# Optimization experiments

Hardware: AMD Instinct MI355X
Metric: run time of the kernel (lower is better)

## Reference

```python
import jax, jax.numpy as jnp
import numpy as np

N_NODES = 100000
N_EDGES = 1600000
IN_DIM = 64
HID = 128
OUT_DIM = 2
N_GRAPHS = 64


def setup_inputs() -> dict:
    key = jax.random.key(0)
    ks = jax.random.split(key, 9)
    x = jax.random.normal(ks[0], (N_NODES, IN_DIM), dtype=jnp.float32)
    edge_index = jax.random.randint(ks[1], (2, N_EDGES), 0, N_NODES, dtype=jnp.int64)
    batch = jnp.sort(jax.random.randint(ks[2], (N_NODES,), 0, N_GRAPHS, dtype=jnp.int64))
    # GCNConv weights (Glorot-ish scale) and biases
    W1 = jax.random.normal(ks[3], (IN_DIM, HID), dtype=jnp.float32) / np.sqrt(IN_DIM)
    b1 = jnp.zeros((HID,), dtype=jnp.float32)
    W2 = jax.random.normal(ks[4], (HID, HID), dtype=jnp.float32) / np.sqrt(HID)
    b2 = jnp.zeros((HID,), dtype=jnp.float32)
    Wfc = jax.random.normal(ks[5], (HID, OUT_DIM), dtype=jnp.float32) / np.sqrt(HID)
    bfc = jnp.zeros((OUT_DIM,), dtype=jnp.float32)
    return {"x": x, "W1": W1, "b1": b1, "W2": W2, "b2": b2,
            "Wfc": Wfc, "bfc": bfc, "edge_index": edge_index, "batch": batch}


def _gcn_conv(x, W, b, src, dst, num_nodes):
    # PyG GCNConv: linear transform, add self loops, symmetric deg norm, scatter-add.
    h = x @ W  # [N, F]
    loop = jnp.arange(num_nodes, dtype=src.dtype)
    s = jnp.concatenate([src, loop])  # source (message origin)
    d = jnp.concatenate([dst, loop])  # target (aggregation)
    deg = jax.ops.segment_sum(jnp.ones_like(d, dtype=h.dtype), d, num_segments=num_nodes)
    dinv = jnp.where(deg > 0, jax.lax.rsqrt(deg), 0.0)
    norm = dinv[s] * dinv[d]  # [E+N]
    msg = h[s] * norm[:, None]
    out = jax.ops.segment_sum(msg, d, num_segments=num_nodes)
    return out + b


def reference(x, W1, b1, W2, b2, Wfc, bfc, edge_index, batch):
    src, dst = edge_index[0], edge_index[1]
    n = x.shape[0]
    h = jax.nn.relu(_gcn_conv(x, W1, b1, src, dst, n))
    # dropout is a no-op in eval mode
    h = jax.nn.relu(_gcn_conv(h, W2, b2, src, dst, n))
    # global mean pool over graphs
    sums = jax.ops.segment_sum(h, batch, num_segments=N_GRAPHS)
    cnts = jax.ops.segment_sum(jnp.ones((n,), dtype=h.dtype), batch, num_segments=N_GRAPHS)
    pooled = sums / jnp.maximum(cnts, 1.0)[:, None]  # [G, HID]
    logits = pooled @ Wfc + bfc
    return jax.nn.log_softmax(logits, axis=1)
```

## Files before the change

kernel.cpp:

```cpp
#include <hip/hip_runtime.h>
#include <math.h>

#define N_NODES 100000
#define N_EDGES 1600000
#define IN_DIM 64
#define HID 128
#define OUT_DIM 2
#define N_GRAPHS 64

#define NBUK ((N_NODES + 255) / 256)
#define BCAP 4608
#define E4 (N_EDGES / 4)
#define NBLK_P1 ((E4 + 1023) / 1024)

#define PCHUNK 256
#define MAXCH 8

typedef unsigned int uint32;
typedef __attribute__((ext_vector_type(8))) short bf16x8;
typedef __attribute__((ext_vector_type(4))) float f32x4;

static __device__ __forceinline__ ushort f2bf(float f) {
    uint32 u = __float_as_uint(f);
    uint32 r = (u + 0x7fff + ((u >> 16) & 1)) >> 16;
    return (ushort)r;
}
static __device__ __forceinline__ float bf2f(uint32 u) {
    return __uint_as_float(u << 16);
}
static __device__ __forceinline__ float bflo(uint32 u) { return bf2f(u & 0xffffu); }
static __device__ __forceinline__ float bfhi(uint32 u) { return bf2f(u >> 16); }

__global__ __launch_bounds__(1024) void k_pass1(const int4* __restrict__ src4,
                                                const int4* __restrict__ dst4,
                                                int* __restrict__ gcur,
                                                int* __restrict__ bsrc,
                                                int* __restrict__ bdst) {
    __shared__ int hist[NBUK];
    __shared__ int base[NBUK];
    int tid = threadIdx.x;
    if (tid < NBUK) hist[tid] = 0;
    __syncthreads();
    int i4 = blockIdx.x * 1024 + tid;
    bool act = i4 < E4;
    int4 d = {0, 0, 0, 0}, s = {0, 0, 0, 0};
    if (act) {
        d = dst4[i4];
        s = src4[i4];
        atomicAdd(&hist[d.x >> 8], 1);
        atomicAdd(&hist[d.y >> 8], 1);
        atomicAdd(&hist[d.z >> 8], 1);
        atomicAdd(&hist[d.w >> 8], 1);
    }
    __syncthreads();
    if (tid < NBUK) {
        int c = hist[tid];
        base[tid] = tid * BCAP + (c ? atomicAdd(&gcur[tid], c) : 0);
        hist[tid] = 0;
    }
    __syncthreads();
    if (act) {
        int b0 = d.x >> 8, r0 = atomicAdd(&hist[b0], 1);
        int b1 = d.y >> 8, r1 = atomicAdd(&hist[b1], 1);
        int b2 = d.z >> 8, r2 = atomicAdd(&hist[b2], 1);
        int b3 = d.w >> 8, r3 = atomicAdd(&hist[b3], 1);
        int sl0 = base[b0] + r0;
        int sl1 = base[b1] + r1;
        int sl2 = base[b2] + r2;
        int sl3 = base[b3] + r3;
        bsrc[sl0] = s.x; bdst[sl0] = d.x;
        bsrc[sl1] = s.y; bdst[sl1] = d.y;
        bsrc[sl2] = s.z; bdst[sl2] = d.z;
        bsrc[sl3] = s.w; bdst[sl3] = d.w;
    }
}

__global__ __launch_bounds__(512) void k_bscan(const int* __restrict__ gcur,
                                               int* __restrict__ bstart,
                                               int* __restrict__ row_start) {
    __shared__ int s[512];
    int t = threadIdx.x;
    int v = (t < NBUK) ? gcur[t] : 0;
    s[t] = v;
    __syncthreads();
    for (int off = 1; off < 512; off <<= 1) {
        int u = (t >= off) ? s[t - off] : 0;
        __syncthreads();
        s[t] += u;
        __syncthreads();
    }
    if (t < NBUK) bstart[t] = s[t] - v;
    if (t == 0) row_start[N_NODES] = N_EDGES;
}

__global__ __launch_bounds__(1024) void k_pass2(const int* __restrict__ gcur,
                                                const int* __restrict__ bstart,
                                                const int* __restrict__ bsrc,
                                                const int* __restrict__ bdst,
                                                const float* __restrict__ x,
                                                int* __restrict__ row_start,
                                                float* __restrict__ dinv,
                                                int* __restrict__ csr,
                                                ushort* __restrict__ xs) {
    __shared__ int cnt[256];
    __shared__ int sc[256];
    __shared__ int lst[256];
    __shared__ float sdinv[256];
    int b = blockIdx.x;
    int tid = threadIdx.x;
    int node0 = b * 256;
    int nloc = N_NODES - node0;
    if (nloc > 256) nloc = 256;
    int bbase = b * BCAP;
    int Eb = gcur[b];

    if (tid < 256) cnt[tid] = 0;
    __syncthreads();
    for (int i = tid; i < Eb; i += 1024) atomicAdd(&cnt[bdst[bbase + i] & 255], 1);
    __syncthreads();
    int v = 0;
    if (tid < 256) {
        v = cnt[tid];
        sc[tid] = v;
    }
    __syncthreads();
    for (int off = 1; off < 256; off <<= 1) {
        int u = 0;
        if (tid < 256 && tid >= off) u = sc[tid - off];
        __syncthreads();
        if (tid < 256) sc[tid] += u;
        __syncthreads();
    }
    int gb = bstart[b];
    if (tid < 256) {
        int excl = sc[tid] - v;
        lst[tid] = excl;
        if (tid < nloc) {
            float dv = rsqrtf((float)(v + 1));
            row_start[node0 + tid] = gb + excl;
            dinv[node0 + tid] = dv;
            sdinv[tid] = dv;
        }
        cnt[tid] = 0;
    }
    __syncthreads();
    for (int i = tid; i < Eb; i += 1024) {
        int d = bdst[bbase + i];
        int s = bsrc[bbase + i];
        int dl = d & 255;
        int r = atomicAdd(&cnt[dl], 1);
        csr[gb + lst[dl] + r] = s;
    }
    int f0 = node0 * 16;
    int f1 = (node0 + nloc) * 16;
    for (int idx = f0 + tid; idx < f1; idx += 1024) {
        float dv = sdinv[(idx >> 4) - node0];
        float4 vv = ((const float4*)x)[idx];
        ushort4 o;
        o.x = f2bf(vv.x * dv);
        o.y = f2bf(vv.y * dv);
        o.z = f2bf(vv.z * dv);
        o.w = f2bf(vv.w * dv);
        ((ushort4*)xs)[idx] = o;
    }
}

__global__ __launch_bounds__(256) void k_gbound(const int* __restrict__ batch,
                                                int* __restrict__ gstart) {
    int n = blockIdx.x * 256 + threadIdx.x;
    if (n >= N_NODES) return;
    if (n == 0) {
        for (int g = 0; g <= batch[0]; ++g) gstart[g] = 0;
    } else {
        int a = batch[n - 1], b = batch[n];
        for (int g = a + 1; g <= b; ++g) gstart[g] = n;
    }
    if (n == N_NODES - 1) {
        for (int g = batch[n] + 1; g <= N_GRAPHS; ++g) gstart[g] = N_NODES;
    }
}

__global__ __launch_bounds__(256) void k_agg1(const int* __restrict__ row_start,
                                              const int* __restrict__ csr,
                                              const uint32* __restrict__ xs,
                                              const float* __restrict__ dinv,
                                              uint32* __restrict__ outb) {
    int d = blockIdx.x * 8 + (threadIdx.x >> 5);
    int l = threadIdx.x & 31;
    float dd = dinv[d];
    uint32 u = xs[(long long)d * 32 + l];
    float a0 = bflo(u), a1 = bfhi(u);
    int e = row_start[d];
    int eend = row_start[d + 1];
    for (; e + 7 < eend; e += 8) {
        int s0 = csr[e], s1 = csr[e + 1], s2 = csr[e + 2], s3 = csr[e + 3];
        int s4 = csr[e + 4], s5 = csr[e + 5], s6 = csr[e + 6], s7 = csr[e + 7];
        uint32 w0 = xs[(long long)s0 * 32 + l];
        uint32 w1 = xs[(long long)s1 * 32 + l];
        uint32 w2 = xs[(long long)s2 * 32 + l];
        uint32 w3 = xs[(long long)s3 * 32 + l];
        uint32 w4 = xs[(long long)s4 * 32 + l];
        uint32 w5 = xs[(long long)s5 * 32 + l];
        uint32 w6 = xs[(long long)s6 * 32 + l];
        uint32 w7 = xs[(long long)s7 * 32 + l];
        a0 += ((bflo(w0) + bflo(w1)) + (bflo(w2) + bflo(w3))) +
              ((bflo(w4) + bflo(w5)) + (bflo(w6) + bflo(w7)));
        a1 += ((bfhi(w0) + bfhi(w1)) + (bfhi(w2) + bfhi(w3))) +
              ((bfhi(w4) + bfhi(w5)) + (bfhi(w6) + bfhi(w7)));
    }
    for (; e + 3 < eend; e += 4) {
        int s0 = csr[e], s1 = csr[e + 1], s2 = csr[e + 2], s3 = csr[e + 3];
        uint32 w0 = xs[(long long)s0 * 32 + l];
        uint32 w1 = xs[(long long)s1 * 32 + l];
        uint32 w2 = xs[(long long)s2 * 32 + l];
        uint32 w3 = xs[(long long)s3 * 32 + l];
        a0 += (bflo(w0) + bflo(w1)) + (bflo(w2) + bflo(w3));
        a1 += (bfhi(w0) + bfhi(w1)) + (bfhi(w2) + bfhi(w3));
    }
    for (; e < eend; ++e) {
        uint32 w = xs[(long long)csr[e] * 32 + l];
        a0 += bflo(w);
        a1 += bfhi(w);
    }
    outb[(long long)d * 32 + l] = (uint32)f2bf(a0 * dd) | ((uint32)f2bf(a1 * dd) << 16);
}

__global__ __launch_bounds__(256) void k_agg2(const int* __restrict__ row_start,
                                              const int* __restrict__ csr,
                                              const uint2* __restrict__ hs,
                                              const float* __restrict__ dinv,
                                              uint2* __restrict__ outb) {
    int d = blockIdx.x * 8 + (threadIdx.x >> 5);
    int l = threadIdx.x & 31;
    float dd = dinv[d];
    uint2 u = hs[(long long)d * 32 + l];
    float a0 = bflo(u.x), a1 = bfhi(u.x), a2 = bflo(u.y), a3 = bfhi(u.y);
    int e = row_start[d];
    int eend = row_start[d + 1];
    for (; e + 7 < eend; e += 8) {
        int s0 = csr[e], s1 = csr[e + 1], s2 = csr[e + 2], s3 = csr[e + 3];
        int s4 = csr[e + 4], s5 = csr[e + 5], s6 = csr[e + 6], s7 = csr[e + 7];
        uint2 w0 = hs[(long long)s0 * 32 + l];
        uint2 w1 = hs[(long long)s1 * 32 + l];
        uint2 w2 = hs[(long long)s2 * 32 + l];
        uint2 w3 = hs[(long long)s3 * 32 + l];
        uint2 w4 = hs[(long long)s4 * 32 + l];
        uint2 w5 = hs[(long long)s5 * 32 + l];
        uint2 w6 = hs[(long long)s6 * 32 + l];
        uint2 w7 = hs[(long long)s7 * 32 + l];
        a0 += ((bflo(w0.x) + bflo(w1.x)) + (bflo(w2.x) + bflo(w3.x))) +
              ((bflo(w4.x) + bflo(w5.x)) + (bflo(w6.x) + bflo(w7.x)));
        a1 += ((bfhi(w0.x) + bfhi(w1.x)) + (bfhi(w2.x) + bfhi(w3.x))) +
              ((bfhi(w4.x) + bfhi(w5.x)) + (bfhi(w6.x) + bfhi(w7.x)));
        a2 += ((bflo(w0.y) + bflo(w1.y)) + (bflo(w2.y) + bflo(w3.y))) +
              ((bflo(w4.y) + bflo(w5.y)) + (bflo(w6.y) + bflo(w7.y)));
        a3 += ((bfhi(w0.y) + bfhi(w1.y)) + (bfhi(w2.y) + bfhi(w3.y))) +
              ((bfhi(w4.y) + bfhi(w5.y)) + (bfhi(w6.y) + bfhi(w7.y)));
    }
    for (; e + 3 < eend; e += 4) {
        int s0 = csr[e], s1 = csr[e + 1], s2 = csr[e + 2], s3 = csr[e + 3];
        uint2 w0 = hs[(long long)s0 * 32 + l];
        uint2 w1 = hs[(long long)s1 * 32 + l];
        uint2 w2 = hs[(long long)s2 * 32 + l];
        uint2 w3 = hs[(long long)s3 * 32 + l];
        a0 += (bflo(w0.x) + bflo(w1.x)) + (bflo(w2.x) + bflo(w3.x));
        a1 += (bfhi(w0.x) + bfhi(w1.x)) + (bfhi(w2.x) + bfhi(w3.x));
        a2 += (bflo(w0.y) + bflo(w1.y)) + (bflo(w2.y) + bflo(w3.y));
        a3 += (bfhi(w0.y) + bfhi(w1.y)) + (bfhi(w2.y) + bfhi(w3.y));
    }
    for (; e < eend; ++e) {
        uint2 w = hs[(long long)csr[e] * 32 + l];
        a0 += bflo(w.x);
        a1 += bfhi(w.x);
        a2 += bflo(w.y);
        a3 += bfhi(w.y);
    }
    uint2 o;
    o.x = (uint32)f2bf(a0 * dd) | ((uint32)f2bf(a1 * dd) << 16);
    o.y = (uint32)f2bf(a2 * dd) | ((uint32)f2bf(a3 * dd) << 16);
    outb[(long long)d * 32 + l] = o;
}

template <int K, int OUTM>
__global__ __launch_bounds__(256) void k_gemm_mfma(const ushort* __restrict__ A,
                                                   const float* __restrict__ W,
                                                   const float* __restrict__ bias,
                                                   const float* __restrict__ dinv,
                                                   void* __restrict__ outv) {
    constexpr int KSTEPS = K / 32;
    constexpr int LDSK = K + 8;
    __shared__ ushort WT[128 * LDSK];
    int tid = threadIdx.x;
    for (int idx = tid; idx < K * 128; idx += 256) {
        int k = idx >> 7, c = idx & 127;
        WT[c * LDSK + k] = f2bf(W[idx]);
    }
    __syncthreads();

    int w = tid >> 6, l = tid & 63;
    int row0 = blockIdx.x * 64 + w * 16;
    int arow = row0 + (l & 15);
    if (arow > N_NODES - 1) arow = N_NODES - 1;
    int koff = (l >> 4) * 8;

    bf16x8 af[KSTEPS];
#pragma unroll
    for (int ks = 0; ks < KSTEPS; ++ks)
        af[ks] = *(const bf16x8*)(A + (long long)arow * K + ks * 32 + koff);

    f32x4 acc[8];
#pragma unroll
    for (int t = 0; t < 8; ++t) acc[t] = (f32x4){0.f, 0.f, 0.f, 0.f};

#pragma unroll
    for (int ks = 0; ks < KSTEPS; ++ks) {
#pragma unroll
        for (int t = 0; t < 8; ++t) {
            int c = t * 16 + (l & 15);
            bf16x8 bf = *(const bf16x8*)&WT[c * LDSK + ks * 32 + koff];
            acc[t] = __builtin_amdgcn_mfma_f32_16x16x32_bf16(af[ks], bf, acc[t], 0, 0, 0);
        }
    }

    int rbase = row0 + ((l >> 4) << 2);
#pragma unroll
    for (int t = 0; t < 8; ++t) {
        int col = t * 16 + (l & 15);
        float bb = bias[col];
#pragma unroll
        for (int i = 0; i < 4; ++i) {
            int row = rbase + i;
            if (row < N_NODES) {
                float v = acc[t][i] + bb;
                v = v > 0.f ? v : 0.f;
                if (OUTM == 1) {
                    ((ushort*)outv)[(long long)row * HID + col] = f2bf(v * dinv[row]);
                } else if (OUTM == 2) {
                    ((ushort*)outv)[(long long)row * HID + col] = f2bf(v);
                } else {
                    ((float*)outv)[(long long)row * HID + col] = v;
                }
            }
        }
    }
}

__global__ __launch_bounds__(256) void k_pool(const uint32* __restrict__ h2,
                                              const int* __restrict__ gstart,
                                              float* __restrict__ pooled) {
    int g = blockIdx.x >> 3;
    int c = blockIdx.x & (MAXCH - 1);
    int r0 = gstart[g] + c * PCHUNK;
    int r1 = gstart[g + 1];
    if (r0 >= r1) return;
    int rend = r0 + PCHUNK;
    if (rend > r1) rend = r1;
    int j = threadIdx.x & 63;
    int q = threadIdx.x >> 6;
    float a0 = 0.f, a1 = 0.f, b0 = 0.f, b1 = 0.f;
    int r = r0 + q;
    for (; r + 4 < rend; r += 8) {
        uint32 u = h2[(long long)r * 64 + j];
        uint32 v = h2[(long long)(r + 4) * 64 + j];
        a0 += bflo(u);
        a1 += bfhi(u);
        b0 += bflo(v);
        b1 += bfhi(v);
    }
    for (; r < rend; r += 4) {
        uint32 u = h2[(long long)r * 64 + j];
        a0 += bflo(u);
        a1 += bfhi(u);
    }
    __shared__ float red[256][2];
    red[threadIdx.x][0] = a0 + b0;
    red[threadIdx.x][1] = a1 + b1;
    __syncthreads();
    if (q == 0) {
        float s0 = (red[j][0] + red[j + 64][0]) + (red[j + 128][0] + red[j + 192][0]);
        float s1 = (red[j][1] + red[j + 64][1]) + (red[j + 128][1] + red[j + 192][1]);
        atomicAdd(&pooled[g * HID + 2 * j], s0);
        atomicAdd(&pooled[g * HID + 2 * j + 1], s1);
    }
}

__global__ __launch_bounds__(256) void k_head(const float* __restrict__ pooled,
                                              const int* __restrict__ gstart,
                                              const float* __restrict__ Wfc,
                                              const float* __restrict__ bfc,
                                              float* __restrict__ out) {
    int t = threadIdx.x;
    int g = t >> 2, sub = t & 3;
    float inv = 1.0f / fmaxf((float)(gstart[g + 1] - gstart[g]), 1.0f);
    float l0 = 0.f, l1 = 0.f;
    for (int j = sub * 32; j < sub * 32 + 32; ++j) {
        float p = pooled[g * HID + j] * inv;
        l0 += p * Wfc[j * OUT_DIM + 0];
        l1 += p * Wfc[j * OUT_DIM + 1];
    }
    l0 += __shfl_xor(l0, 1);
    l1 += __shfl_xor(l1, 1);
    l0 += __shfl_xor(l0, 2);
    l1 += __shfl_xor(l1, 2);
    if (sub == 0) {
        l0 += bfc[0];
        l1 += bfc[1];
        float m = fmaxf(l0, l1);
        float lse = m + logf(expf(l0 - m) + expf(l1 - m));
        out[g * OUT_DIM + 0] = l0 - lse;
        out[g * OUT_DIM + 1] = l1 - lse;
    }
}

extern "C" void kernel_launch(void* const* d_in, const int* in_sizes, int n_in,
                              void* d_out, int out_size, void* d_ws, size_t ws_size,
                              hipStream_t stream) {
    const float* x   = (const float*)d_in[0];
    const float* W1  = (const float*)d_in[1];
    const float* b1  = (const float*)d_in[2];
    const float* W2  = (const float*)d_in[3];
    const float* b2  = (const float*)d_in[4];
    const float* Wfc = (const float*)d_in[5];
    const float* bfc = (const float*)d_in[6];
    const int* ei    = (const int*)d_in[7];
    const int* batch = (const int*)d_in[8];
    const int* src = ei;
    const int* dst = ei + N_EDGES;
    float* out = (float*)d_out;

    float* bufA = (float*)d_ws;
    float* bufB = bufA + (long long)N_NODES * HID;
    int* bsrc = (int*)bufA;
    int* bdst = bsrc + NBUK * BCAP;
    ushort* agg1o = (ushort*)bufA;
    ushort* agg2o = (ushort*)bufA;
    ushort* xs = (ushort*)bufB;
    ushort* hs = (ushort*)bufB;
    ushort* h2 = (ushort*)bufB;
    int* row_start = (int*)(bufB + (long long)N_NODES * HID);
    float* dinv = (float*)(row_start + N_NODES + 1);
    int* gcur = (int*)(dinv + N_NODES);
    int* bstart = gcur + NBUK;
    int* gstart = bstart + NBUK;
    int* csr = gstart + (N_GRAPHS + 1);
    float* pooled = (float*)(csr + N_EDGES);

    hipMemsetAsync(gcur, 0, NBUK * sizeof(int), stream);
    hipMemsetAsync(pooled, 0, N_GRAPHS * HID * sizeof(float), stream);
    k_pass1<<<NBLK_P1, 1024, 0, stream>>>((const int4*)src, (const int4*)dst, gcur, bsrc, bdst);
    k_bscan<<<1, 512, 0, stream>>>(gcur, bstart, row_start);
    k_pass2<<<NBUK, 1024, 0, stream>>>(gcur, bstart, bsrc, bdst, x, row_start, dinv, csr, xs);
    k_gbound<<<(N_NODES + 255) / 256, 256, 0, stream>>>(batch, gstart);

    const int NGBLK = (N_NODES + 63) / 64;

    k_agg1<<<N_NODES / 8, 256, 0, stream>>>(row_start, csr, (const uint32*)xs, dinv,
                                            (uint32*)agg1o);
    k_gemm_mfma<IN_DIM, 1><<<NGBLK, 256, 0, stream>>>(agg1o, W1, b1, dinv, hs);

    k_agg2<<<N_NODES / 8, 256, 0, stream>>>(row_start, csr, (const uint2*)hs, dinv,
                                            (uint2*)agg2o);
    k_gemm_mfma<HID, 2><<<NGBLK, 256, 0, stream>>>(agg2o, W2, b2, dinv, h2);

    k_pool<<<N_GRAPHS * MAXCH, 256, 0, stream>>>((const uint32*)h2, gstart, pooled);
    k_head<<<1, 256, 0, stream>>>(pooled, gstart, Wfc, bfc, out);
}
```

Baseline: 218.3 us.

## Fuse aggregation into MFMA GEMM, pack edge buckets, fold bucket scan into pass2

Each GCN layer now runs the neighbour aggregation and the MFMA GEMM in one kernel. The aggregated rows are staged in LDS instead of being written to and reread from global memory. Edge bucketing packs the local dst byte and src index into a single int, which halves bucket traffic. The separate bucket-offset scan kernel is replaced by a redundant scan inside each pass2 block. The trade-offs are that each block does 8 nodes per warp-group serially before the GEMM, which may lower latency hiding, and that the packing assumes src fits in 24 bits.

```diff
diff --git a/kernel.cpp b/kernel.cpp
--- a/kernel.cpp
+++ b/kernel.cpp
@@ -30,12 +30,14 @@
 }
 static __device__ __forceinline__ float bflo(uint32 u) { return bf2f(u & 0xffffu); }
 static __device__ __forceinline__ float bfhi(uint32 u) { return bf2f(u >> 16); }
+static __device__ __forceinline__ uint32 pack2(float a, float b) {
+    return (uint32)f2bf(a) | ((uint32)f2bf(b) << 16);
+}
 
 __global__ __launch_bounds__(1024) void k_pass1(const int4* __restrict__ src4,
                                                 const int4* __restrict__ dst4,
                                                 int* __restrict__ gcur,
-                                                int* __restrict__ bsrc,
-                                                int* __restrict__ bdst) {
+                                                int* __restrict__ bpak) {
     __shared__ int hist[NBUK];
     __shared__ int base[NBUK];
     int tid = threadIdx.x;
@@ -64,39 +66,15 @@
         int b1 = d.y >> 8, r1 = atomicAdd(&hist[b1], 1);
         int b2 = d.z >> 8, r2 = atomicAdd(&hist[b2], 1);
         int b3 = d.w >> 8, r3 = atomicAdd(&hist[b3], 1);
-        int sl0 = base[b0] + r0;
-        int sl1 = base[b1] + r1;
-        int sl2 = base[b2] + r2;
-        int sl3 = base[b3] + r3;
-        bsrc[sl0] = s.x; bdst[sl0] = d.x;
-        bsrc[sl1] = s.y; bdst[sl1] = d.y;
-        bsrc[sl2] = s.z; bdst[sl2] = d.z;
-        bsrc[sl3] = s.w; bdst[sl3] = d.w;
-    }
-}
-
-__global__ __launch_bounds__(512) void k_bscan(const int* __restrict__ gcur,
-                                               int* __restrict__ bstart,
-                                               int* __restrict__ row_start) {
-    __shared__ int s[512];
-    int t = threadIdx.x;
-    int v = (t < NBUK) ? gcur[t] : 0;
-    s[t] = v;
-    __syncthreads();
-    for (int off = 1; off < 512; off <<= 1) {
-        int u = (t >= off) ? s[t - off] : 0;
-        __syncthreads();
-        s[t] += u;
-        __syncthreads();
-    }
-    if (t < NBUK) bstart[t] = s[t] - v;
-    if (t == 0) row_start[N_NODES] = N_EDGES;
+        bpak[base[b0] + r0] = ((d.x & 255) << 24) | s.x;
+        bpak[base[b1] + r1] = ((d.y & 255) << 24) | s.y;
+        bpak[base[b2] + r2] = ((d.z & 255) << 24) | s.z;
+        bpak[base[b3] + r3] = ((d.w & 255) << 24) | s.w;
+    }
 }
 
 __global__ __launch_bounds__(1024) void k_pass2(const int* __restrict__ gcur,
-                                                const int* __restrict__ bstart,
-                                                const int* __restrict__ bsrc,
-                                                const int* __restrict__ bdst,
+                                                const int* __restrict__ bpak,
                                                 const float* __restrict__ x,
                                                 int* __restrict__ row_start,
                                                 float* __restrict__ dinv,
@@ -106,6 +84,8 @@
     __shared__ int sc[256];
     __shared__ int lst[256];
     __shared__ float sdinv[256];
+    __shared__ int sg[1024];
+    __shared__ int sgb;
     int b = blockIdx.x;
     int tid = threadIdx.x;
     int node0 = b * 256;
@@ -114,9 +94,20 @@
     int bbase = b * BCAP;
     int Eb = gcur[b];
 
+    sg[tid] = (tid < NBUK) ? gcur[tid] : 0;
     if (tid < 256) cnt[tid] = 0;
     __syncthreads();
-    for (int i = tid; i < Eb; i += 1024) atomicAdd(&cnt[bdst[bbase + i] & 255], 1);
+    for (int off = 1; off < 512; off <<= 1) {
+        int u = (tid >= off) ? sg[tid - off] : 0;
+        __syncthreads();
+        sg[tid] += u;
+        __syncthreads();
+    }
+    if (tid == 0) sgb = (b == 0) ? 0 : sg[b - 1];
+    __syncthreads();
+    int gb = sgb;
+
+    for (int i = tid; i < Eb; i += 1024) atomicAdd(&cnt[(uint32)bpak[bbase + i] >> 24], 1);
     __syncthreads();
     int v = 0;
     if (tid < 256) {
@@ -131,7 +122,6 @@
         if (tid < 256) sc[tid] += u;
         __syncthreads();
     }
-    int gb = bstart[b];
     if (tid < 256) {
         int excl = sc[tid] - v;
         lst[tid] = excl;
@@ -145,11 +135,10 @@
     }
     __syncthreads();
     for (int i = tid; i < Eb; i += 1024) {
-        int d = bdst[bbase + i];
-        int s = bsrc[bbase + i];
-        int dl = d & 255;
+        int p = bpak[bbase + i];
+        int dl = (uint32)p >> 24;
         int r = atomicAdd(&cnt[dl], 1);
-        csr[gb + lst[dl] + r] = s;
+        csr[gb + lst[dl] + r] = p & 0xFFFFFF;
     }
     int f0 = node0 * 16;
     int f1 = (node0 + nloc) * 16;
@@ -166,7 +155,8 @@
 }
 
 __global__ __launch_bounds__(256) void k_gbound(const int* __restrict__ batch,
-                                                int* __restrict__ gstart) {
+                                                int* __restrict__ gstart,
+                                                int* __restrict__ row_start) {
     int n = blockIdx.x * 256 + threadIdx.x;
     if (n >= N_NODES) return;
     if (n == 0) {
@@ -177,136 +167,126 @@
     }
     if (n == N_NODES - 1) {
         for (int g = batch[n] + 1; g <= N_GRAPHS; ++g) gstart[g] = N_NODES;
-    }
-}
-
-__global__ __launch_bounds__(256) void k_agg1(const int* __restrict__ row_start,
-                                              const int* __restrict__ csr,
-                                              const uint32* __restrict__ xs,
-                                              const float* __restrict__ dinv,
-                                              uint32* __restrict__ outb) {
-    int d = blockIdx.x * 8 + (threadIdx.x >> 5);
-    int l = threadIdx.x & 31;
-    float dd = dinv[d];
-    uint32 u = xs[(long long)d * 32 + l];
-    float a0 = bflo(u), a1 = bfhi(u);
-    int e = row_start[d];
-    int eend = row_start[d + 1];
-    for (; e + 7 < eend; e += 8) {
-        int s0 = csr[e], s1 = csr[e + 1], s2 = csr[e + 2], s3 = csr[e + 3];
-        int s4 = csr[e + 4], s5 = csr[e + 5], s6 = csr[e + 6], s7 = csr[e + 7];
-        uint32 w0 = xs[(long long)s0 * 32 + l];
-        uint32 w1 = xs[(long long)s1 * 32 + l];
-        uint32 w2 = xs[(long long)s2 * 32 + l];
-        uint32 w3 = xs[(long long)s3 * 32 + l];
-        uint32 w4 = xs[(long long)s4 * 32 + l];
-        uint32 w5 = xs[(long long)s5 * 32 + l];
-        uint32 w6 = xs[(long long)s6 * 32 + l];
-        uint32 w7 = xs[(long long)s7 * 32 + l];
-        a0 += ((bflo(w0) + bflo(w1)) + (bflo(w2) + bflo(w3))) +
-              ((bflo(w4) + bflo(w5)) + (bflo(w6) + bflo(w7)));
-        a1 += ((bfhi(w0) + bfhi(w1)) + (bfhi(w2) + bfhi(w3))) +
-              ((bfhi(w4) + bfhi(w5)) + (bfhi(w6) + bfhi(w7)));
-    }
-    for (; e + 3 < eend; e += 4) {
-        int s0 = csr[e], s1 = csr[e + 1], s2 = csr[e + 2], s3 = csr[e + 3];
-        uint32 w0 = xs[(long long)s0 * 32 + l];
-        uint32 w1 = xs[(long long)s1 * 32 + l];
-        uint32 w2 = xs[(long long)s2 * 32 + l];
-        uint32 w3 = xs[(long long)s3 * 32 + l];
-        a0 += (bflo(w0) + bflo(w1)) + (bflo(w2) + bflo(w3));
-        a1 += (bfhi(w0) + bfhi(w1)) + (bfhi(w2) + bfhi(w3));
-    }
-    for (; e < eend; ++e) {
-        uint32 w = xs[(long long)csr[e] * 32 + l];
-        a0 += bflo(w);
-        a1 += bfhi(w);
-    }
-    outb[(long long)d * 32 + l] = (uint32)f2bf(a0 * dd) | ((uint32)f2bf(a1 * dd) << 16);
-}
-
-__global__ __launch_bounds__(256) void k_agg2(const int* __restrict__ row_start,
-                                              const int* __restrict__ csr,
-                                              const uint2* __restrict__ hs,
-                                              const float* __restrict__ dinv,
-                                              uint2* __restrict__ outb) {
-    int d = blockIdx.x * 8 + (threadIdx.x >> 5);
-    int l = threadIdx.x & 31;
-    float dd = dinv[d];
-    uint2 u = hs[(long long)d * 32 + l];
-    float a0 = bflo(u.x), a1 = bfhi(u.x), a2 = bflo(u.y), a3 = bfhi(u.y);
-    int e = row_start[d];
-    int eend = row_start[d + 1];
-    for (; e + 7 < eend; e += 8) {
-        int s0 = csr[e], s1 = csr[e + 1], s2 = csr[e + 2], s3 = csr[e + 3];
-        int s4 = csr[e + 4], s5 = csr[e + 5], s6 = csr[e + 6], s7 = csr[e + 7];
-        uint2 w0 = hs[(long long)s0 * 32 + l];
-        uint2 w1 = hs[(long long)s1 * 32 + l];
-        uint2 w2 = hs[(long long)s2 * 32 + l];
-        uint2 w3 = hs[(long long)s3 * 32 + l];
-        uint2 w4 = hs[(long long)s4 * 32 + l];
-        uint2 w5 = hs[(long long)s5 * 32 + l];
-        uint2 w6 = hs[(long long)s6 * 32 + l];
-        uint2 w7 = hs[(long long)s7 * 32 + l];
-        a0 += ((bflo(w0.x) + bflo(w1.x)) + (bflo(w2.x) + bflo(w3.x))) +
-              ((bflo(w4.x) + bflo(w5.x)) + (bflo(w6.x) + bflo(w7.x)));
-        a1 += ((bfhi(w0.x) + bfhi(w1.x)) + (bfhi(w2.x) + bfhi(w3.x))) +
-              ((bfhi(w4.x) + bfhi(w5.x)) + (bfhi(w6.x) + bfhi(w7.x)));
-        a2 += ((bflo(w0.y) + bflo(w1.y)) + (bflo(w2.y) + bflo(w3.y))) +
-              ((bflo(w4.y) + bflo(w5.y)) + (bflo(w6.y) + bflo(w7.y)));
-        a3 += ((bfhi(w0.y) + bfhi(w1.y)) + (bfhi(w2.y) + bfhi(w3.y))) +
-              ((bfhi(w4.y) + bfhi(w5.y)) + (bfhi(w6.y) + bfhi(w7.y)));
-    }
-    for (; e + 3 < eend; e += 4) {
-        int s0 = csr[e], s1 = csr[e + 1], s2 = csr[e + 2], s3 = csr[e + 3];
-        uint2 w0 = hs[(long long)s0 * 32 + l];
-        uint2 w1 = hs[(long long)s1 * 32 + l];
-        uint2 w2 = hs[(long long)s2 * 32 + l];
-        uint2 w3 = hs[(long long)s3 * 32 + l];
-        a0 += (bflo(w0.x) + bflo(w1.x)) + (bflo(w2.x) + bflo(w3.x));
-        a1 += (bfhi(w0.x) + bfhi(w1.x)) + (bfhi(w2.x) + bfhi(w3.x));
-        a2 += (bflo(w0.y) + bflo(w1.y)) + (bflo(w2.y) + bflo(w3.y));
-        a3 += (bfhi(w0.y) + bfhi(w1.y)) + (bfhi(w2.y) + bfhi(w3.y));
-    }
-    for (; e < eend; ++e) {
-        uint2 w = hs[(long long)csr[e] * 32 + l];
-        a0 += bflo(w.x);
-        a1 += bfhi(w.x);
-        a2 += bflo(w.y);
-        a3 += bfhi(w.y);
-    }
-    uint2 o;
-    o.x = (uint32)f2bf(a0 * dd) | ((uint32)f2bf(a1 * dd) << 16);
-    o.y = (uint32)f2bf(a2 * dd) | ((uint32)f2bf(a3 * dd) << 16);
-    outb[(long long)d * 32 + l] = o;
+        row_start[N_NODES] = N_EDGES;
+    }
 }
 
 template <int K, int OUTM>
-__global__ __launch_bounds__(256) void k_gemm_mfma(const ushort* __restrict__ A,
-                                                   const float* __restrict__ W,
-                                                   const float* __restrict__ bias,
-                                                   const float* __restrict__ dinv,
-                                                   void* __restrict__ outv) {
+__global__ __launch_bounds__(256) void k_fused(const int* __restrict__ row_start,
+                                               const int* __restrict__ csr,
+                                               const ushort* __restrict__ table,
+                                               const float* __restrict__ dinv,
+                                               const float* __restrict__ W,
+                                               const float* __restrict__ bias,
+                                               ushort* __restrict__ outb) {
     constexpr int KSTEPS = K / 32;
     constexpr int LDSK = K + 8;
     __shared__ ushort WT[128 * LDSK];
+    __shared__ ushort AT[64 * LDSK];
     int tid = threadIdx.x;
     for (int idx = tid; idx < K * 128; idx += 256) {
         int k = idx >> 7, c = idx & 127;
         WT[c * LDSK + k] = f2bf(W[idx]);
     }
-    __syncthreads();
-
-    int w = tid >> 6, l = tid & 63;
-    int row0 = blockIdx.x * 64 + w * 16;
-    int arow = row0 + (l & 15);
-    if (arow > N_NODES - 1) arow = N_NODES - 1;
-    int koff = (l >> 4) * 8;
+
+    int grp = tid >> 5, l = tid & 31;
+    for (int n8 = 0; n8 < 8; ++n8) {
+        int nl = grp * 8 + n8;
+        int node = blockIdx.x * 64 + nl;
+        if constexpr (K == 64) {
+            const uint32* tb = (const uint32*)table;
+            float a0 = 0.f, a1 = 0.f;
+            if (node < N_NODES) {
+                float dd = dinv[node];
+                uint32 u = tb[(long long)node * 32 + l];
+                a0 = bflo(u);
+                a1 = bfhi(u);
+                int e = row_start[node];
+                int eend = row_start[node + 1];
+                for (; e + 7 < eend; e += 8) {
+                    int s0 = csr[e], s1 = csr[e + 1], s2 = csr[e + 2], s3 = csr[e + 3];
+                    int s4 = csr[e + 4], s5 = csr[e + 5], s6 = csr[e + 6], s7 = csr[e + 7];
+                    uint32 w0 = tb[(long long)s0 * 32 + l];
+                    uint32 w1 = tb[(long long)s1 * 32 + l];
+                    uint32 w2 = tb[(long long)s2 * 32 + l];
+                    uint32 w3 = tb[(long long)s3 * 32 + l];
+                    uint32 w4 = tb[(long long)s4 * 32 + l];
+                    uint32 w5 = tb[(long long)s5 * 32 + l];
+                    uint32 w6 = tb[(long long)s6 * 32 + l];
+                    uint32 w7 = tb[(long long)s7 * 32 + l];
+                    a0 += ((bflo(w0) + bflo(w1)) + (bflo(w2) + bflo(w3))) +
+                          ((bflo(w4) + bflo(w5)) + (bflo(w6) + bflo(w7)));
+                    a1 += ((bfhi(w0) + bfhi(w1)) + (bfhi(w2) + bfhi(w3))) +
+                          ((bfhi(w4) + bfhi(w5)) + (bfhi(w6) + bfhi(w7)));
+                }
+                for (; e < eend; ++e) {
+                    uint32 w = tb[(long long)csr[e] * 32 + l];
+                    a0 += bflo(w);
+                    a1 += bfhi(w);
+                }
+                a0 *= dd;
+                a1 *= dd;
+            }
+            ((uint32*)AT)[nl * (LDSK / 2) + l] = pack2(a0, a1);
+        } else {
+            const uint2* tb = (const uint2*)table;
+            float a0 = 0.f, a1 = 0.f, a2 = 0.f, a3 = 0.f;
+            if (node < N_NODES) {
+                float dd = dinv[node];
+                uint2 u = tb[(long long)node * 32 + l];
+                a0 = bflo(u.x);
+                a1 = bfhi(u.x);
+                a2 = bflo(u.y);
+                a3 = bfhi(u.y);
+                int e = row_start[node];
+                int eend = row_start[node + 1];
+                for (; e + 7 < eend; e += 8) {
+                    int s0 = csr[e], s1 = csr[e + 1], s2 = csr[e + 2], s3 = csr[e + 3];
+                    int s4 = csr[e + 4], s5 = csr[e + 5], s6 = csr[e + 6], s7 = csr[e + 7];
+                    uint2 w0 = tb[(long long)s0 * 32 + l];
+                    uint2 w1 = tb[(long long)s1 * 32 + l];
+                    uint2 w2 = tb[(long long)s2 * 32 + l];
+                    uint2 w3 = tb[(long long)s3 * 32 + l];
+                    uint2 w4 = tb[(long long)s4 * 32 + l];
+                    uint2 w5 = tb[(long long)s5 * 32 + l];
+                    uint2 w6 = tb[(long long)s6 * 32 + l];
+                    uint2 w7 = tb[(long long)s7 * 32 + l];
+                    a0 += ((bflo(w0.x) + bflo(w1.x)) + (bflo(w2.x) + bflo(w3.x))) +
+                          ((bflo(w4.x) + bflo(w5.x)) + (bflo(w6.x) + bflo(w7.x)));
+                    a1 += ((bfhi(w0.x) + bfhi(w1.x)) + (bfhi(w2.x) + bfhi(w3.x))) +
+                          ((bfhi(w4.x) + bfhi(w5.x)) + (bfhi(w6.x) + bfhi(w7.x)));
+                    a2 += ((bflo(w0.y) + bflo(w1.y)) + (bflo(w2.y) + bflo(w3.y))) +
+                          ((bflo(w4.y) + bflo(w5.y)) + (bflo(w6.y) + bflo(w7.y)));
+                    a3 += ((bfhi(w0.y) + bfhi(w1.y)) + (bfhi(w2.y) + bfhi(w3.y))) +
+                          ((bfhi(w4.y) + bfhi(w5.y)) + (bfhi(w6.y) + bfhi(w7.y)));
+                }
+                for (; e < eend; ++e) {
+                    uint2 w = tb[(long long)csr[e] * 32 + l];
+                    a0 += bflo(w.x);
+                    a1 += bfhi(w.x);
+                    a2 += bflo(w.y);
+                    a3 += bfhi(w.y);
+                }
+                a0 *= dd;
+                a1 *= dd;
+                a2 *= dd;
+                a3 *= dd;
+            }
+            uint32* arow = (uint32*)&AT[nl * LDSK];
+            arow[2 * l] = pack2(a0, a1);
+            arow[2 * l + 1] = pack2(a2, a3);
+        }
+    }
+    __syncthreads();
+
+    int w = tid >> 6, l64 = tid & 63;
+    int arow = w * 16 + (l64 & 15);
+    int koff = (l64 >> 4) * 8;
 
     bf16x8 af[KSTEPS];
 #pragma unroll
     for (int ks = 0; ks < KSTEPS; ++ks)
-        af[ks] = *(const bf16x8*)(A + (long long)arow * K + ks * 32 + koff);
+        af[ks] = *(const bf16x8*)&AT[arow * LDSK + ks * 32 + koff];
 
     f32x4 acc[8];
 #pragma unroll
@@ -316,16 +296,16 @@
     for (int ks = 0; ks < KSTEPS; ++ks) {
 #pragma unroll
         for (int t = 0; t < 8; ++t) {
-            int c = t * 16 + (l & 15);
+            int c = t * 16 + (l64 & 15);
             bf16x8 bf = *(const bf16x8*)&WT[c * LDSK + ks * 32 + koff];
             acc[t] = __builtin_amdgcn_mfma_f32_16x16x32_bf16(af[ks], bf, acc[t], 0, 0, 0);
         }
     }
 
-    int rbase = row0 + ((l >> 4) << 2);
+    int rbase = blockIdx.x * 64 + w * 16 + ((l64 >> 4) << 2);
 #pragma unroll
     for (int t = 0; t < 8; ++t) {
-        int col = t * 16 + (l & 15);
+        int col = t * 16 + (l64 & 15);
         float bb = bias[col];
 #pragma unroll
         for (int i = 0; i < 4; ++i) {
@@ -333,13 +313,8 @@
             if (row < N_NODES) {
                 float v = acc[t][i] + bb;
                 v = v > 0.f ? v : 0.f;
-                if (OUTM == 1) {
-                    ((ushort*)outv)[(long long)row * HID + col] = f2bf(v * dinv[row]);
-                } else if (OUTM == 2) {
-                    ((ushort*)outv)[(long long)row * HID + col] = f2bf(v);
-                } else {
-                    ((float*)outv)[(long long)row * HID + col] = v;
-                }
+                if (OUTM == 1) v *= dinv[row];
+                outb[(long long)row * HID + col] = f2bf(v);
             }
         }
     }
@@ -430,37 +405,28 @@
 
     float* bufA = (float*)d_ws;
     float* bufB = bufA + (long long)N_NODES * HID;
-    int* bsrc = (int*)bufA;
-    int* bdst = bsrc + NBUK * BCAP;
-    ushort* agg1o = (ushort*)bufA;
-    ushort* agg2o = (ushort*)bufA;
+    int* bpak = (int*)bufA;
+    ushort* hs = (ushort*)bufA;
     ushort* xs = (ushort*)bufB;
-    ushort* hs = (ushort*)bufB;
     ushort* h2 = (ushort*)bufB;
     int* row_start = (int*)(bufB + (long long)N_NODES * HID);
     float* dinv = (float*)(row_start + N_NODES + 1);
     int* gcur = (int*)(dinv + N_NODES);
-    int* bstart = gcur + NBUK;
-    int* gstart = bstart + NBUK;
+    int* gstart = gcur + NBUK;
     int* csr = gstart + (N_GRAPHS + 1);
     float* pooled = (float*)(csr + N_EDGES);
 
     hipMemsetAsync(gcur, 0, NBUK * sizeof(int), stream);
     hipMemsetAsync(pooled, 0, N_GRAPHS * HID * sizeof(float), stream);
-    k_pass1<<<NBLK_P1, 1024, 0, stream>>>((const int4*)src, (const int4*)dst, gcur, bsrc, bdst);
-    k_bscan<<<1, 512, 0, stream>>>(gcur, bstart, row_start);
-    k_pass2<<<NBUK, 1024, 0, stream>>>(gcur, bstart, bsrc, bdst, x, row_start, dinv, csr, xs);
-    k_gbound<<<(N_NODES + 255) / 256, 256, 0, stream>>>(batch, gstart);
+    k_pass1<<<NBLK_P1, 1024, 0, stream>>>((const int4*)src, (const int4*)dst, gcur, bpak);
+    k_pass2<<<NBUK, 1024, 0, stream>>>(gcur, bpak, x, row_start, dinv, csr, xs);
+    k_gbound<<<(N_NODES + 255) / 256, 256, 0, stream>>>(batch, gstart, row_start);
 
     const int NGBLK = (N_NODES + 63) / 64;
 
-    k_agg1<<<N_NODES / 8, 256, 0, stream>>>(row_start, csr, (const uint32*)xs, dinv,
-                                            (uint32*)agg1o);
-    k_gemm_mfma<IN_DIM, 1><<<NGBLK, 256, 0, stream>>>(agg1o, W1, b1, dinv, hs);
-
-    k_agg2<<<N_NODES / 8, 256, 0, stream>>>(row_start, csr, (const uint2*)hs, dinv,
-                                            (uint2*)agg2o);
-    k_gemm_mfma<HID, 2><<<NGBLK, 256, 0, stream>>>(agg2o, W2, b2, dinv, h2);
+    k_fused<IN_DIM, 1><<<NGBLK, 256, 0, stream>>>(row_start, csr, xs, dinv, W1, b1, hs);
+
+    k_fused<HID, 2><<<NGBLK, 256, 0, stream>>>(row_start, csr, hs, dinv, W2, b2, h2);
 
     k_pool<<<N_GRAPHS * MAXCH, 256, 0, stream>>>((const uint32*)h2, gstart, pooled);
     k_head<<<1, 256, 0, stream>>>(pooled, gstart, Wfc, bfc, out);
```

After: 317.8 us. 45.5% more time.
